# Kernel tuning notes

Measured on AMD Instinct MI355X. Metric: run time of the kernel, lower is better.

## Reference

```python
import jax, jax.numpy as jnp
import numpy as np

N_NODES = 100000
IN_CH, HID_CH, OUT_CH = 128, 128, 64
N_EDGES = 1600000


def gcn_conv(x, W, b, src, dst, num_nodes):
    """PyG GCNConv: x@W -> symmetric-normalized aggregation with self-loops -> +bias."""
    h = x @ W  # [N, out]
    loop = jnp.arange(num_nodes, dtype=src.dtype)
    src_a = jnp.concatenate([src, loop])  # add self-loops
    dst_a = jnp.concatenate([dst, loop])
    # degree of destination nodes over augmented edge set (edge_weight = 1)
    deg = jax.ops.segment_sum(jnp.ones_like(dst_a, dtype=h.dtype), dst_a,
                              num_segments=num_nodes)
    dis = jnp.where(deg > 0, jax.lax.rsqrt(jnp.maximum(deg, 1e-30)), 0.0)
    norm = dis[src_a] * dis[dst_a]  # [E+N]
    msg = h[src_a] * norm[:, None]  # gather + normalize
    out = jax.ops.segment_sum(msg, dst_a, num_segments=num_nodes)  # scatter-add
    return out + b


def setup_inputs() -> dict:
    key = jax.random.key(0)
    ks = jax.random.split(key, 9)
    x = jax.random.normal(ks[0], (N_NODES, IN_CH), dtype=jnp.float32)
    edge_index = jax.random.randint(ks[1], (2, N_EDGES), 0, N_NODES, dtype=jnp.int64)
    def glorot(k, fan_in, fan_out):
        s = np.sqrt(6.0 / (fan_in + fan_out)).astype(np.float32)
        return jax.random.uniform(k, (fan_in, fan_out), jnp.float32, -s, s)
    return {
        "x": x,
        "edge_index": edge_index,
        "W1": glorot(ks[2], IN_CH, HID_CH),
        "b1": jnp.zeros((HID_CH,), jnp.float32),
        "W2": glorot(ks[3], HID_CH, HID_CH),
        "b2": jnp.zeros((HID_CH,), jnp.float32),
        "Wo": glorot(ks[4], HID_CH, OUT_CH),
        "bo": jnp.zeros((OUT_CH,), jnp.float32),
    }


def reference(x, edge_index, W1, b1, W2, b2, Wo, bo):
    src, dst = edge_index[0], edge_index[1]
    n = x.shape[0]
    x1 = jax.nn.relu(gcn_conv(x, W1, b1, src, dst, n))
    x2 = jax.nn.relu(gcn_conv(x1, W2, b2, src, dst, n))
    return (x1 + x2) @ Wo + bo
```

## Files before the change

### kernel.cpp

```cpp
#include <hip/hip_runtime.h>
#include <hip/hip_fp16.h>

#define N_NODES 100000
#define N_EDGES 1600000
#define CH 128
#define OCH 64
#define NBUCKET 391
#define CAP 8192
#define BIN_CHUNK 4096
#define ZROW N_NODES
#define GG 782

typedef _Float16 half8 __attribute__((ext_vector_type(8)));
typedef float f32x4 __attribute__((ext_vector_type(4)));

__device__ __forceinline__ ushort f2h(float f) {
    _Float16 h = (_Float16)f;
    return *(ushort*)&h;
}

__device__ __forceinline__ uint pkadd(uint a, uint b) {
    __half2 r = __hadd2(*(__half2*)&a, *(__half2*)&b);
    return *(uint*)&r;
}

__device__ __forceinline__ uint4 pk4(uint4 a, uint4 b) {
    a.x = pkadd(a.x, b.x); a.y = pkadd(a.y, b.y);
    a.z = pkadd(a.z, b.z); a.w = pkadd(a.w, b.w);
    return a;
}

__device__ __forceinline__ int swz(int row, int k) {
    return row * 128 + ((((k >> 3) ^ (row & 15)) << 3) | (k & 7));
}


__global__ __launch_bounds__(512) void k_bin_prep(const int* __restrict__ src,
                                                  const int* __restrict__ dst,
                                                  int* __restrict__ bfill,
                                                  int* __restrict__ bin,
                                                  const float* __restrict__ W1,
                                                  const float* __restrict__ W2,
                                                  const float* __restrict__ Wo,
                                                  ushort* __restrict__ W1s,
                                                  ushort* __restrict__ W2s,
                                                  ushort* __restrict__ WoTs,
                                                  ushort* __restrict__ h) {
    __shared__ int hist[512];
    __shared__ int excl[512];
    __shared__ int wbase[512];
    __shared__ int cur[512];
    __shared__ int sbuf[BIN_CHUNK];
    __shared__ ushort sbkt[BIN_CHUNK];
    const int t = threadIdx.x;

    if (blockIdx.x >= NBUCKET) {
        int b = blockIdx.x - NBUCKET;
        if (b == 80) {
            if (t < CH) h[(size_t)ZROW * CH + t] = 0;
        } else {
            int i = b * 512 + t;
            if (i < 16384) {
                int k = i >> 7, n = i & 127;
                W1s[swz(n, k)] = f2h(W1[i]);
            } else if (i < 32768) {
                int j = i - 16384, k = j >> 7, n = j & 127;
                W2s[swz(n, k)] = f2h(W2[j]);
            } else {
                int j = i - 32768, k = j >> 6, n = j & 63;
                WoTs[swz(n, k)] = f2h(Wo[j]);
            }
        }
        return;
    }

    const int e0 = blockIdx.x * BIN_CHUNK;
    hist[t] = 0;
    __syncthreads();

    int ss[8], bb[8], dl[8];
#pragma unroll
    for (int j = 0; j < 8; ++j) {
        int e = e0 + j * 512 + t;
        bb[j] = -1;
        if (e < N_EDGES) {
            int s = src[e], d = dst[e];
            ss[j] = s; dl[j] = d & 255; bb[j] = d >> 8;
            atomicAdd(&hist[bb[j]], 1);
        }
    }
    __syncthreads();

    int v = hist[t];
    for (int off = 1; off < 512; off <<= 1) {
        int tv = (t >= off) ? hist[t - off] : 0;
        __syncthreads();
        hist[t] += tv;
        __syncthreads();
    }
    int ex = hist[t] - v;
    excl[t] = ex;
    cur[t] = ex;
    if (t < NBUCKET && v > 0) wbase[t] = atomicAdd(&bfill[t], v);
    __syncthreads();

#pragma unroll
    for (int j = 0; j < 8; ++j) {
        if (bb[j] >= 0) {
            int p = atomicAdd(&cur[bb[j]], 1);
            sbuf[p] = (ss[j] << 8) | dl[j];
            sbkt[p] = (ushort)bb[j];
        }
    }
    const int nloc = hist[511];
    __syncthreads();

    for (int i = t; i < nloc; i += 512) {
        int b = sbkt[i];
        bin[b * CAP + wbase[b] + (i - excl[b])] = sbuf[i];
    }
}


__global__ __launch_bounds__(512) void k_build(const int* __restrict__ bfill,
                                               const int* __restrict__ bin,
                                               int* __restrict__ esrc,
                                               int2* __restrict__ scnt,
                                               float* __restrict__ dis) {
    __shared__ int pre[512];
    __shared__ int cnt_l[256];
    __shared__ int cur_l[256];
    __shared__ int sortbuf[CAP];
    const int t = threadIdx.x;
    const int b = blockIdx.x;

    pre[t] = (t < NBUCKET) ? bfill[t] : 0;
    if (t < 256) cnt_l[t] = 0;
    __syncthreads();
    for (int off = 1; off < 512; off <<= 1) {
        int tv = (t >= off) ? pre[t - off] : 0;
        __syncthreads();
        pre[t] += tv;
        __syncthreads();
    }
    const int n = bfill[b];
    const int base = pre[b] - n;
    const int* brec = bin + b * CAP;

    for (int i = t; i < n; i += 512)
        atomicAdd(&cnt_l[brec[i] & 255], 1);
    __syncthreads();

    int v = (t < 256) ? cnt_l[t] : 0;
    for (int off = 1; off < 256; off <<= 1) {
        int tv = (t >= off && t < 256) ? cnt_l[t - off] : 0;
        __syncthreads();
        if (t < 256) cnt_l[t] += tv;
        __syncthreads();
    }
    if (t < 256) {
        int excl = cnt_l[t] - v;
        int node = b * 256 + t;
        if (node < N_NODES) {
            scnt[node] = make_int2(base + excl, v);
            dis[node] = rsqrtf((float)(v + 1));
        }
        cur_l[t] = excl;
    }
    __syncthreads();

    for (int i = t; i < n; i += 512) {
        int rec = brec[i];
        int p = atomicAdd(&cur_l[rec & 255], 1);
        sortbuf[p] = rec >> 8;
    }
    __syncthreads();
    for (int i = t; i < n; i += 512)
        esrc[base + i] = sortbuf[i];
}


template <typename IT>
__global__ __launch_bounds__(512) void k_gemm_mfma(const IT* __restrict__ A,
                                                   const ushort* __restrict__ Ws,
                                                   const float* __restrict__ dis,
                                                   ushort* __restrict__ out) {
    __shared__ ushort sB[128 * 128];
    __shared__ ushort sA[128 * 136];
    const int tid = threadIdx.x;
    const int row0 = blockIdx.x * 128;

    for (int i = tid; i < 2048; i += 512)
        ((float4*)sB)[i] = ((const float4*)Ws)[i];

    for (int i = tid; i < 4096; i += 512) {
        int m = i >> 5, u = i & 31, k4 = u << 2;
        int r = row0 + m;
        ushort4 pk = make_ushort4(0, 0, 0, 0);
        if (r < N_NODES) {
            if constexpr (sizeof(IT) == 4) {
                float4 a = ((const float4*)A)[r * 32 + u];
                pk = make_ushort4(f2h(a.x), f2h(a.y), f2h(a.z), f2h(a.w));
            } else {
                pk = ((const ushort4*)A)[r * 32 + u];
            }
        }
        *(ushort4*)&sA[swz(m, k4)] = pk;
    }
    __syncthreads();

    const int lane = tid & 63, wv = tid >> 6;
    const int mrow = lane & 15, quad = lane >> 4;
    f32x4 acc[8] = {};
#pragma unroll
    for (int kc = 0; kc < 4; ++kc) {
        int g = kc * 4 + quad;
        half8 a = *(const half8*)&sA[(wv * 16 + mrow) * 128 + ((g ^ mrow) << 3)];
#pragma unroll
        for (int nt = 0; nt < 8; ++nt) {
            half8 b = *(const half8*)&sB[(nt * 16 + mrow) * 128 + ((g ^ mrow) << 3)];
            acc[nt] = __builtin_amdgcn_mfma_f32_16x16x32_f16(a, b, acc[nt], 0, 0, 0);
        }
    }

    const int rbase4 = wv * 16 + quad * 4;
    float ds[4];
#pragma unroll
    for (int rg = 0; rg < 4; ++rg) {
        int r = row0 + rbase4 + rg;
        ds[rg] = (r < N_NODES) ? dis[r] : 0.f;
    }

    __syncthreads();
#pragma unroll
    for (int nt = 0; nt < 8; ++nt) {
#pragma unroll
        for (int rg = 0; rg < 4; ++rg)
            sA[(rbase4 + rg) * 136 + nt * 16 + mrow] = f2h(acc[nt][rg] * ds[rg]);
    }
    __syncthreads();

#pragma unroll
    for (int k = 0; k < 4; ++k) {
        int idx = tid + k * 512;
        int m = idx >> 4, c16 = idx & 15;
        int r = row0 + m;
        if (r < N_NODES) {
            uint4 vv = *(const uint4*)&sA[m * 136 + c16 * 8];
            ((uint4*)out)[(size_t)r * 16 + c16] = vv;
        }
    }
}


struct Ictx { int n; int grp; int s0, s1, s2, s3, s4, s5; };
struct Gt { uint4 t0, t1, t2, t3, t4, t5, slf; };

__device__ __forceinline__ Ictx idx_stage(const int* __restrict__ esrc, int off, int n, int q) {
    Ictx c; c.n = n;
    const int* ep = esrc + off;
    int r0 = ep[q], r1 = ep[q + 4], r2 = ep[q + 8];
    int r3 = ep[q + 12], r4 = ep[q + 16], r5 = ep[q + 20];
    bool grp = (q + 12 < n);
    bool ok = (n <= q + 24);
    c.grp = grp;
    c.s0 = (grp || q < n)      ? r0 : ZROW;
    c.s1 = (grp || q + 4 < n)  ? r1 : ZROW;
    c.s2 = (grp || q + 8 < n)  ? r2 : ZROW;
    c.s3 = grp                 ? r3 : ZROW;
    c.s4 = (grp && ok && q + 16 < n) ? r4 : ZROW;
    c.s5 = (grp && ok && q + 20 < n) ? r5 : ZROW;
    return c;
}

__device__ __forceinline__ Gt gather_stage(const Ictx& c, int v, int l,
                                           const uint4* __restrict__ h16) {
    Gt g;
    g.t0 = h16[(size_t)c.s0 * 16 + l];
    g.t1 = h16[(size_t)c.s1 * 16 + l];
    g.t2 = h16[(size_t)c.s2 * 16 + l];
    g.t3 = h16[(size_t)c.s3 * 16 + l];
    g.t4 = h16[(size_t)c.s4 * 16 + l];
    g.t5 = h16[(size_t)c.s5 * 16 + l];
    g.slf = h16[(size_t)v * 16 + l];
    return g;
}

__device__ __forceinline__ void acc_finish(const Gt& g, const Ictx& c, int v, int q, int l,
                                           const int* __restrict__ esrc, int off,
                                           const uint4* __restrict__ h16,
                                           float dsv, float4 b0, float4 b1,
                                           ushort* __restrict__ out) {
    uint4 aA = make_uint4(0, 0, 0, 0), aB = make_uint4(0, 0, 0, 0);
    aA = pk4(aA, g.t0);
    if (c.grp) aB = pk4(aB, g.t1); else aA = pk4(aA, g.t1);
    aA = pk4(aA, g.t2);
    if (c.grp) aB = pk4(aB, g.t3); else aA = pk4(aA, g.t3);
    aA = pk4(aA, g.t4);
    aA = pk4(aA, g.t5);
    if (c.n > q + 24) {
        const int* ep = esrc + off;
        int i = q + 16;
        for (; i + 12 < c.n; i += 16) {
            uint4 u0 = h16[(size_t)ep[i] * 16 + l];
            uint4 u1 = h16[(size_t)ep[i + 4] * 16 + l];
            uint4 u2 = h16[(size_t)ep[i + 8] * 16 + l];
            uint4 u3 = h16[(size_t)ep[i + 12] * 16 + l];
            aA = pk4(aA, u0); aB = pk4(aB, u1); aA = pk4(aA, u2); aB = pk4(aB, u3);
        }
        for (; i < c.n; i += 4) aA = pk4(aA, h16[(size_t)ep[i] * 16 + l]);
    }
    aA = pk4(aA, aB);
    aA.x = pkadd(aA.x, (uint)__shfl_xor((int)aA.x, 16));
    aA.y = pkadd(aA.y, (uint)__shfl_xor((int)aA.y, 16));
    aA.z = pkadd(aA.z, (uint)__shfl_xor((int)aA.z, 16));
    aA.w = pkadd(aA.w, (uint)__shfl_xor((int)aA.w, 16));
    aA.x = pkadd(aA.x, (uint)__shfl_xor((int)aA.x, 32));
    aA.y = pkadd(aA.y, (uint)__shfl_xor((int)aA.y, 32));
    aA.z = pkadd(aA.z, (uint)__shfl_xor((int)aA.z, 32));
    aA.w = pkadd(aA.w, (uint)__shfl_xor((int)aA.w, 32));

    if (q == 0) {
        aA = pk4(aA, g.slf);
        float2 a0 = __half22float2(*(__half2*)&aA.x);
        float2 a1 = __half22float2(*(__half2*)&aA.y);
        float2 a2 = __half22float2(*(__half2*)&aA.z);
        float2 a3 = __half22float2(*(__half2*)&aA.w);
        a0.x = fmaxf(a0.x * dsv + b0.x, 0.f); a0.y = fmaxf(a0.y * dsv + b0.y, 0.f);
        a1.x = fmaxf(a1.x * dsv + b0.z, 0.f); a1.y = fmaxf(a1.y * dsv + b0.w, 0.f);
        a2.x = fmaxf(a2.x * dsv + b1.x, 0.f); a2.y = fmaxf(a2.y * dsv + b1.y, 0.f);
        a3.x = fmaxf(a3.x * dsv + b1.z, 0.f); a3.y = fmaxf(a3.y * dsv + b1.w, 0.f);
        __half2 o0 = __float22half2_rn(a0);
        __half2 o1 = __float22half2_rn(a1);
        __half2 o2 = __float22half2_rn(a2);
        __half2 o3 = __float22half2_rn(a3);
        ((uint4*)out)[v * 16 + l] =
            make_uint4(*(uint*)&o0, *(uint*)&o1, *(uint*)&o2, *(uint*)&o3);
    }
}

__global__ __launch_bounds__(256) void k_agg(const int2* __restrict__ scnt,
                                             const int* __restrict__ esrc,
                                             const ushort* __restrict__ h,
                                             const float* __restrict__ dis,
                                             const float* __restrict__ bias,
                                             ushort* __restrict__ out) {
    const int w = threadIdx.x >> 6;
    const int vb = blockIdx.x * 16 + w * 4;
    const int lane = threadIdx.x & 63, q = lane >> 4, l = lane & 15;
    const uint4* h16 = (const uint4*)h;

    int2 m0 = scnt[vb], m1 = scnt[vb + 1], m2 = scnt[vb + 2], m3 = scnt[vb + 3];
    float d0 = dis[vb], d1 = dis[vb + 1], d2 = dis[vb + 2], d3 = dis[vb + 3];
    float4 b0 = ((const float4*)bias)[2 * l];
    float4 b1 = ((const float4*)bias)[2 * l + 1];

    Ictx c0 = idx_stage(esrc, m0.x, m0.y, q);
    Gt g0 = gather_stage(c0, vb, l, h16);
    Ictx c1 = idx_stage(esrc, m1.x, m1.y, q);
    Gt g1 = gather_stage(c1, vb + 1, l, h16);
    Ictx c2 = idx_stage(esrc, m2.x, m2.y, q);
    acc_finish(g0, c0, vb, q, l, esrc, m0.x, h16, d0, b0, b1, out);
    Gt g2 = gather_stage(c2, vb + 2, l, h16);
    Ictx c3 = idx_stage(esrc, m3.x, m3.y, q);
    acc_finish(g1, c1, vb + 1, q, l, esrc, m1.x, h16, d1, b0, b1, out);
    Gt g3 = gather_stage(c3, vb + 3, l, h16);
    acc_finish(g2, c2, vb + 2, q, l, esrc, m2.x, h16, d2, b0, b1, out);
    acc_finish(g3, c3, vb + 3, q, l, esrc, m3.x, h16, d3, b0, b1, out);
}


__global__ __launch_bounds__(512) void k_final_mfma(const ushort* __restrict__ x1,
                                                    const ushort* __restrict__ x2,
                                                    const ushort* __restrict__ Ws,
                                                    const float* __restrict__ bo,
                                                    float* __restrict__ out) {
    __shared__ ushort sB[64 * 128];
    __shared__ float sF[128 * 68];
    ushort* sA = (ushort*)sF;
    const int tid = threadIdx.x;
    const int row0 = blockIdx.x * 128;

    for (int i = tid; i < 1024; i += 512)
        ((float4*)sB)[i] = ((const float4*)Ws)[i];

    for (int i = tid; i < 4096; i += 512) {
        int m = i >> 5, u = i & 31, k4 = u << 2;
        int r = row0 + m;
        uint2 pk = make_uint2(0, 0);
        if (r < N_NODES) {
            uint2 ua = ((const uint2*)x1)[r * 32 + u];
            uint2 ub = ((const uint2*)x2)[r * 32 + u];
            __half2 s0 = __hadd2(*(__half2*)&ua.x, *(__half2*)&ub.x);
            __half2 s1 = __hadd2(*(__half2*)&ua.y, *(__half2*)&ub.y);
            pk = make_uint2(*(uint*)&s0, *(uint*)&s1);
        }
        *(uint2*)&sA[swz(m, k4)] = pk;
    }
    __syncthreads();

    const int lane = tid & 63, wv = tid >> 6;
    const int mrow = lane & 15, quad = lane >> 4;
    f32x4 acc[4] = {};
#pragma unroll
    for (int kc = 0; kc < 4; ++kc) {
        int g = kc * 4 + quad;
        half8 a = *(const half8*)&sA[(wv * 16 + mrow) * 128 + ((g ^ mrow) << 3)];
#pragma unroll
        for (int nt = 0; nt < 4; ++nt) {
            half8 b = *(const half8*)&sB[(nt * 16 + mrow) * 128 + ((g ^ mrow) << 3)];
            acc[nt] = __builtin_amdgcn_mfma_f32_16x16x32_f16(a, b, acc[nt], 0, 0, 0);
        }
    }

    const int rbase4 = wv * 16 + quad * 4;
    __syncthreads();
#pragma unroll
    for (int nt = 0; nt < 4; ++nt) {
        float bb = bo[nt * 16 + mrow];
#pragma unroll
        for (int rg = 0; rg < 4; ++rg)
            sF[(rbase4 + rg) * 68 + nt * 16 + mrow] = acc[nt][rg] + bb;
    }
    __syncthreads();

#pragma unroll
    for (int k = 0; k < 4; ++k) {
        int idx = tid + k * 512;
        int m = idx >> 4, c16 = idx & 15;
        int r = row0 + m;
        if (r < N_NODES) {
            uint4 vv = *(const uint4*)&sF[m * 68 + c16 * 4];
            ((uint4*)out)[(size_t)r * 16 + c16] = vv;
        }
    }
}


extern "C" void kernel_launch(void* const* d_in, const int* in_sizes, int n_in,
                              void* d_out, int out_size, void* d_ws, size_t ws_size,
                              hipStream_t stream) {
    const float* x  = (const float*)d_in[0];
    const int*   ei = (const int*)d_in[1];
    const int*   src = ei;
    const int*   dst = ei + N_EDGES;
    const float* W1 = (const float*)d_in[2];
    const float* b1 = (const float*)d_in[3];
    const float* W2 = (const float*)d_in[4];
    const float* b2 = (const float*)d_in[5];
    const float* Wo = (const float*)d_in[6];
    const float* bo = (const float*)d_in[7];
    float* out = (float*)d_out;

    char* ws = (char*)d_ws;
    int*    bfill  = (int*)ws;            ws += 2048;
    int2*   scnt   = (int2*)ws;           ws += 800000;
    float*  dis    = (float*)ws;          ws += 400000;
    int*    bin    = (int*)ws;            ws += (size_t)NBUCKET * CAP * 4;
    int*    esrc   = (int*)ws;            ws += (size_t)N_EDGES * 4;
    ushort* W1s    = (ushort*)ws;         ws += 32768;
    ushort* W2s    = (ushort*)ws;         ws += 32768;
    ushort* WoTs   = (ushort*)ws;         ws += 16384;
    ushort* h      = (ushort*)ws;         ws += (size_t)(N_NODES + 1) * CH * 2;
    ushort* x1     = (ushort*)ws;         ws += (size_t)N_NODES * CH * 2;
    ushort* x2     = (ushort*)ws;

    const int gA = N_NODES / 16;

    hipMemsetAsync(bfill, 0, 2048, stream);
    k_bin_prep<<<NBUCKET + 81, 512, 0, stream>>>(src, dst, bfill, bin,
                                                 W1, W2, Wo, W1s, W2s, WoTs, h);
    k_build<<<NBUCKET, 512, 0, stream>>>(bfill, bin, esrc, scnt, dis);

    k_gemm_mfma<float><<<GG, 512, 0, stream>>>(x, W1s, dis, h);
    k_agg<<<gA, 256, 0, stream>>>(scnt, esrc, h, dis, b1, x1);

    k_gemm_mfma<ushort><<<GG, 512, 0, stream>>>(x1, W2s, dis, h);
    k_agg<<<gA, 256, 0, stream>>>(scnt, esrc, h, dis, b2, x2);

    k_final_mfma<<<GG, 512, 0, stream>>>(x1, x2, WoTs, bo, out);
}
```

Before: 297.7 us.

## Fuse aggregation with following GEMMs to drop intermediate round-trips

The first aggregation kernel now also multiplies its 16-row output tile by W2 with MFMA and writes the dis-scaled h2 directly, which removes the separate second GEMM launch. The second aggregation fuses the x1 residual add and the output projection by Wo plus bias, which removes the x2 buffer and the final GEMM kernel. This saves two launches and the global write and reread of x2 and of x1 for the GEMM. In exchange the W2 and Wo fragments are read from global memory by every small block instead of being staged in LDS, and each block's MFMA work is small.

```diff
diff --git a/kernel.cpp b/kernel.cpp
--- a/kernel.cpp
+++ b/kernel.cpp
@@ -45,7 +45,8 @@
                                                   ushort* __restrict__ W1s,
                                                   ushort* __restrict__ W2s,
                                                   ushort* __restrict__ WoTs,
-                                                  ushort* __restrict__ h) {
+                                                  ushort* __restrict__ h,
+                                                  ushort* __restrict__ h2) {
     __shared__ int hist[512];
     __shared__ int excl[512];
     __shared__ int wbase[512];
@@ -57,7 +58,10 @@
     if (blockIdx.x >= NBUCKET) {
         int b = blockIdx.x - NBUCKET;
         if (b == 80) {
-            if (t < CH) h[(size_t)ZROW * CH + t] = 0;
+            if (t < CH) {
+                h[(size_t)ZROW * CH + t] = 0;
+                h2[(size_t)ZROW * CH + t] = 0;
+            }
         } else {
             int i = b * 512 + t;
             if (i < 16384) {
@@ -180,8 +184,7 @@
 }
 
 
-template <typename IT>
-__global__ __launch_bounds__(512) void k_gemm_mfma(const IT* __restrict__ A,
+__global__ __launch_bounds__(512) void k_gemm_mfma(const float* __restrict__ A,
                                                    const ushort* __restrict__ Ws,
                                                    const float* __restrict__ dis,
                                                    ushort* __restrict__ out) {
@@ -198,12 +201,8 @@
         int r = row0 + m;
         ushort4 pk = make_ushort4(0, 0, 0, 0);
         if (r < N_NODES) {
-            if constexpr (sizeof(IT) == 4) {
-                float4 a = ((const float4*)A)[r * 32 + u];
-                pk = make_ushort4(f2h(a.x), f2h(a.y), f2h(a.z), f2h(a.w));
-            } else {
-                pk = ((const ushort4*)A)[r * 32 + u];
-            }
+            float4 a = ((const float4*)A)[r * 32 + u];
+            pk = make_ushort4(f2h(a.x), f2h(a.y), f2h(a.z), f2h(a.w));
         }
         *(ushort4*)&sA[swz(m, k4)] = pk;
     }
@@ -286,11 +285,10 @@
     return g;
 }
 
-__device__ __forceinline__ void acc_finish(const Gt& g, const Ictx& c, int v, int q, int l,
-                                           const int* __restrict__ esrc, int off,
-                                           const uint4* __restrict__ h16,
-                                           float dsv, float4 b0, float4 b1,
-                                           ushort* __restrict__ out) {
+__device__ __forceinline__ uint4 acc_reduce(const Gt& g, const Ictx& c, int q, int l,
+                                            const int* __restrict__ esrc, int off,
+                                            const uint4* __restrict__ h16,
+                                            float dsv, float4 b0, float4 b1) {
     uint4 aA = make_uint4(0, 0, 0, 0), aB = make_uint4(0, 0, 0, 0);
     aA = pk4(aA, g.t0);
     if (c.grp) aB = pk4(aB, g.t1); else aA = pk4(aA, g.t1);
@@ -320,34 +318,38 @@
     aA.z = pkadd(aA.z, (uint)__shfl_xor((int)aA.z, 32));
     aA.w = pkadd(aA.w, (uint)__shfl_xor((int)aA.w, 32));
 
-    if (q == 0) {
-        aA = pk4(aA, g.slf);
-        float2 a0 = __half22float2(*(__half2*)&aA.x);
-        float2 a1 = __half22float2(*(__half2*)&aA.y);
-        float2 a2 = __half22float2(*(__half2*)&aA.z);
-        float2 a3 = __half22float2(*(__half2*)&aA.w);
-        a0.x = fmaxf(a0.x * dsv + b0.x, 0.f); a0.y = fmaxf(a0.y * dsv + b0.y, 0.f);
-        a1.x = fmaxf(a1.x * dsv + b0.z, 0.f); a1.y = fmaxf(a1.y * dsv + b0.w, 0.f);
-        a2.x = fmaxf(a2.x * dsv + b1.x, 0.f); a2.y = fmaxf(a2.y * dsv + b1.y, 0.f);
-        a3.x = fmaxf(a3.x * dsv + b1.z, 0.f); a3.y = fmaxf(a3.y * dsv + b1.w, 0.f);
-        __half2 o0 = __float22half2_rn(a0);
-        __half2 o1 = __float22half2_rn(a1);
-        __half2 o2 = __float22half2_rn(a2);
-        __half2 o3 = __float22half2_rn(a3);
-        ((uint4*)out)[v * 16 + l] =
-            make_uint4(*(uint*)&o0, *(uint*)&o1, *(uint*)&o2, *(uint*)&o3);
-    }
-}
-
-__global__ __launch_bounds__(256) void k_agg(const int2* __restrict__ scnt,
-                                             const int* __restrict__ esrc,
-                                             const ushort* __restrict__ h,
-                                             const float* __restrict__ dis,
-                                             const float* __restrict__ bias,
-                                             ushort* __restrict__ out) {
-    const int w = threadIdx.x >> 6;
-    const int vb = blockIdx.x * 16 + w * 4;
-    const int lane = threadIdx.x & 63, q = lane >> 4, l = lane & 15;
+    aA = pk4(aA, g.slf);
+    float2 a0 = __half22float2(*(__half2*)&aA.x);
+    float2 a1 = __half22float2(*(__half2*)&aA.y);
+    float2 a2 = __half22float2(*(__half2*)&aA.z);
+    float2 a3 = __half22float2(*(__half2*)&aA.w);
+    a0.x = fmaxf(a0.x * dsv + b0.x, 0.f); a0.y = fmaxf(a0.y * dsv + b0.y, 0.f);
+    a1.x = fmaxf(a1.x * dsv + b0.z, 0.f); a1.y = fmaxf(a1.y * dsv + b0.w, 0.f);
+    a2.x = fmaxf(a2.x * dsv + b1.x, 0.f); a2.y = fmaxf(a2.y * dsv + b1.y, 0.f);
+    a3.x = fmaxf(a3.x * dsv + b1.z, 0.f); a3.y = fmaxf(a3.y * dsv + b1.w, 0.f);
+    __half2 o0 = __float22half2_rn(a0);
+    __half2 o1 = __float22half2_rn(a1);
+    __half2 o2 = __float22half2_rn(a2);
+    __half2 o3 = __float22half2_rn(a3);
+    return make_uint4(*(uint*)&o0, *(uint*)&o1, *(uint*)&o2, *(uint*)&o3);
+}
+
+
+__global__ __launch_bounds__(256) void k_agg_gemm(const int2* __restrict__ scnt,
+                                                  const int* __restrict__ esrc,
+                                                  const ushort* __restrict__ h,
+                                                  const float* __restrict__ dis,
+                                                  const float* __restrict__ bias,
+                                                  const ushort* __restrict__ W2s,
+                                                  ushort* __restrict__ x1,
+                                                  ushort* __restrict__ h2) {
+    __shared__ ushort tile[16 * 128];
+    __shared__ ushort sBnc[16 * 136];
+    const int t = threadIdx.x;
+    const int w = t >> 6;
+    const int vb0 = blockIdx.x * 16;
+    const int vb = vb0 + w * 4;
+    const int lane = t & 63, q = lane >> 4, l = lane & 15;
     const uint4* h16 = (const uint4*)h;
 
     int2 m0 = scnt[vb], m1 = scnt[vb + 1], m2 = scnt[vb + 2], m3 = scnt[vb + 3];
@@ -360,80 +362,124 @@
     Ictx c1 = idx_stage(esrc, m1.x, m1.y, q);
     Gt g1 = gather_stage(c1, vb + 1, l, h16);
     Ictx c2 = idx_stage(esrc, m2.x, m2.y, q);
-    acc_finish(g0, c0, vb, q, l, esrc, m0.x, h16, d0, b0, b1, out);
+    uint4 ov = acc_reduce(g0, c0, q, l, esrc, m0.x, h16, d0, b0, b1);
+    if (q == 0) {
+        ((uint4*)x1)[(size_t)vb * 16 + l] = ov;
+        *(uint4*)&tile[swz(w * 4 + 0, l * 8)] = ov;
+    }
     Gt g2 = gather_stage(c2, vb + 2, l, h16);
     Ictx c3 = idx_stage(esrc, m3.x, m3.y, q);
-    acc_finish(g1, c1, vb + 1, q, l, esrc, m1.x, h16, d1, b0, b1, out);
+    ov = acc_reduce(g1, c1, q, l, esrc, m1.x, h16, d1, b0, b1);
+    if (q == 0) {
+        ((uint4*)x1)[(size_t)(vb + 1) * 16 + l] = ov;
+        *(uint4*)&tile[swz(w * 4 + 1, l * 8)] = ov;
+    }
     Gt g3 = gather_stage(c3, vb + 3, l, h16);
-    acc_finish(g2, c2, vb + 2, q, l, esrc, m2.x, h16, d2, b0, b1, out);
-    acc_finish(g3, c3, vb + 3, q, l, esrc, m3.x, h16, d3, b0, b1, out);
-}
-
-
-__global__ __launch_bounds__(512) void k_final_mfma(const ushort* __restrict__ x1,
-                                                    const ushort* __restrict__ x2,
-                                                    const ushort* __restrict__ Ws,
-                                                    const float* __restrict__ bo,
-                                                    float* __restrict__ out) {
-    __shared__ ushort sB[64 * 128];
-    __shared__ float sF[128 * 68];
-    ushort* sA = (ushort*)sF;
-    const int tid = threadIdx.x;
-    const int row0 = blockIdx.x * 128;
-
-    for (int i = tid; i < 1024; i += 512)
-        ((float4*)sB)[i] = ((const float4*)Ws)[i];
-
-    for (int i = tid; i < 4096; i += 512) {
-        int m = i >> 5, u = i & 31, k4 = u << 2;
-        int r = row0 + m;
-        uint2 pk = make_uint2(0, 0);
-        if (r < N_NODES) {
-            uint2 ua = ((const uint2*)x1)[r * 32 + u];
-            uint2 ub = ((const uint2*)x2)[r * 32 + u];
-            __half2 s0 = __hadd2(*(__half2*)&ua.x, *(__half2*)&ub.x);
-            __half2 s1 = __hadd2(*(__half2*)&ua.y, *(__half2*)&ub.y);
-            pk = make_uint2(*(uint*)&s0, *(uint*)&s1);
-        }
-        *(uint2*)&sA[swz(m, k4)] = pk;
-    }
-    __syncthreads();
-
-    const int lane = tid & 63, wv = tid >> 6;
+    ov = acc_reduce(g2, c2, q, l, esrc, m2.x, h16, d2, b0, b1);
+    if (q == 0) {
+        ((uint4*)x1)[(size_t)(vb + 2) * 16 + l] = ov;
+        *(uint4*)&tile[swz(w * 4 + 2, l * 8)] = ov;
+    }
+    ov = acc_reduce(g3, c3, q, l, esrc, m3.x, h16, d3, b0, b1);
+    if (q == 0) {
+        ((uint4*)x1)[(size_t)(vb + 3) * 16 + l] = ov;
+        *(uint4*)&tile[swz(w * 4 + 3, l * 8)] = ov;
+    }
+    __syncthreads();
+
     const int mrow = lane & 15, quad = lane >> 4;
-    f32x4 acc[4] = {};
+    f32x4 acc0 = {}, acc1 = {};
+    const int nt0 = 2 * w, nt1 = 2 * w + 1;
 #pragma unroll
     for (int kc = 0; kc < 4; ++kc) {
         int g = kc * 4 + quad;
-        half8 a = *(const half8*)&sA[(wv * 16 + mrow) * 128 + ((g ^ mrow) << 3)];
-#pragma unroll
-        for (int nt = 0; nt < 4; ++nt) {
-            half8 b = *(const half8*)&sB[(nt * 16 + mrow) * 128 + ((g ^ mrow) << 3)];
-            acc[nt] = __builtin_amdgcn_mfma_f32_16x16x32_f16(a, b, acc[nt], 0, 0, 0);
-        }
-    }
-
-    const int rbase4 = wv * 16 + quad * 4;
-    __syncthreads();
-#pragma unroll
-    for (int nt = 0; nt < 4; ++nt) {
-        float bb = bo[nt * 16 + mrow];
-#pragma unroll
-        for (int rg = 0; rg < 4; ++rg)
-            sF[(rbase4 + rg) * 68 + nt * 16 + mrow] = acc[nt][rg] + bb;
-    }
-    __syncthreads();
-
-#pragma unroll
-    for (int k = 0; k < 4; ++k) {
-        int idx = tid + k * 512;
-        int m = idx >> 4, c16 = idx & 15;
-        int r = row0 + m;
-        if (r < N_NODES) {
-            uint4 vv = *(const uint4*)&sF[m * 68 + c16 * 4];
-            ((uint4*)out)[(size_t)r * 16 + c16] = vv;
-        }
-    }
+        half8 a = *(const half8*)&tile[mrow * 128 + ((g ^ mrow) << 3)];
+        half8 bf0 = *(const half8*)&W2s[(nt0 * 16 + mrow) * 128 + ((g ^ mrow) << 3)];
+        half8 bf1 = *(const half8*)&W2s[(nt1 * 16 + mrow) * 128 + ((g ^ mrow) << 3)];
+        acc0 = __builtin_amdgcn_mfma_f32_16x16x32_f16(a, bf0, acc0, 0, 0, 0);
+        acc1 = __builtin_amdgcn_mfma_f32_16x16x32_f16(a, bf1, acc1, 0, 0, 0);
+    }
+    float ds[4];
+#pragma unroll
+    for (int rg = 0; rg < 4; ++rg)
+        ds[rg] = dis[vb0 + quad * 4 + rg];
+#pragma unroll
+    for (int rg = 0; rg < 4; ++rg) {
+        sBnc[(quad * 4 + rg) * 136 + nt0 * 16 + mrow] = f2h(acc0[rg] * ds[rg]);
+        sBnc[(quad * 4 + rg) * 136 + nt1 * 16 + mrow] = f2h(acc1[rg] * ds[rg]);
+    }
+    __syncthreads();
+
+    int row = t >> 4, c16 = t & 15;
+    uint4 vv = *(const uint4*)&sBnc[row * 136 + c16 * 8];
+    ((uint4*)h2)[(size_t)(vb0 + row) * 16 + c16] = vv;
+}
+
+
+__global__ __launch_bounds__(256) void k_agg_out(const int2* __restrict__ scnt,
+                                                 const int* __restrict__ esrc,
+                                                 const ushort* __restrict__ h2,
+                                                 const float* __restrict__ dis,
+                                                 const float* __restrict__ bias,
+                                                 const ushort* __restrict__ WoTs,
+                                                 const float* __restrict__ bo,
+                                                 const ushort* __restrict__ x1,
+                                                 float* __restrict__ out) {
+    __shared__ ushort tile[16 * 128];
+    __shared__ float sOut[16 * 68];
+    const int t = threadIdx.x;
+    const int w = t >> 6;
+    const int vb0 = blockIdx.x * 16;
+    const int vb = vb0 + w * 4;
+    const int lane = t & 63, q = lane >> 4, l = lane & 15;
+    const uint4* h16 = (const uint4*)h2;
+    const uint4* x1q = (const uint4*)x1;
+
+    int2 m0 = scnt[vb], m1 = scnt[vb + 1], m2 = scnt[vb + 2], m3 = scnt[vb + 3];
+    float d0 = dis[vb], d1 = dis[vb + 1], d2 = dis[vb + 2], d3 = dis[vb + 3];
+    float4 b0 = ((const float4*)bias)[2 * l];
+    float4 b1 = ((const float4*)bias)[2 * l + 1];
+
+    Ictx c0 = idx_stage(esrc, m0.x, m0.y, q);
+    Gt g0 = gather_stage(c0, vb, l, h16);
+    uint4 xr0 = x1q[(size_t)vb * 16 + l];
+    Ictx c1 = idx_stage(esrc, m1.x, m1.y, q);
+    Gt g1 = gather_stage(c1, vb + 1, l, h16);
+    uint4 xr1 = x1q[(size_t)(vb + 1) * 16 + l];
+    Ictx c2 = idx_stage(esrc, m2.x, m2.y, q);
+    uint4 ov = acc_reduce(g0, c0, q, l, esrc, m0.x, h16, d0, b0, b1);
+    if (q == 0) *(uint4*)&tile[swz(w * 4 + 0, l * 8)] = pk4(ov, xr0);
+    Gt g2 = gather_stage(c2, vb + 2, l, h16);
+    uint4 xr2 = x1q[(size_t)(vb + 2) * 16 + l];
+    Ictx c3 = idx_stage(esrc, m3.x, m3.y, q);
+    uint4 xr3 = x1q[(size_t)(vb + 3) * 16 + l];
+    ov = acc_reduce(g1, c1, q, l, esrc, m1.x, h16, d1, b0, b1);
+    if (q == 0) *(uint4*)&tile[swz(w * 4 + 1, l * 8)] = pk4(ov, xr1);
+    Gt g3 = gather_stage(c3, vb + 3, l, h16);
+    ov = acc_reduce(g2, c2, q, l, esrc, m2.x, h16, d2, b0, b1);
+    if (q == 0) *(uint4*)&tile[swz(w * 4 + 2, l * 8)] = pk4(ov, xr2);
+    ov = acc_reduce(g3, c3, q, l, esrc, m3.x, h16, d3, b0, b1);
+    if (q == 0) *(uint4*)&tile[swz(w * 4 + 3, l * 8)] = pk4(ov, xr3);
+    __syncthreads();
+
+    const int mrow = lane & 15, quad = lane >> 4;
+    f32x4 acc = {};
+#pragma unroll
+    for (int kc = 0; kc < 4; ++kc) {
+        int g = kc * 4 + quad;
+        half8 a = *(const half8*)&tile[mrow * 128 + ((g ^ mrow) << 3)];
+        half8 bf = *(const half8*)&WoTs[(w * 16 + mrow) * 128 + ((g ^ mrow) << 3)];
+        acc = __builtin_amdgcn_mfma_f32_16x16x32_f16(a, bf, acc, 0, 0, 0);
+    }
+    float bb = bo[w * 16 + mrow];
+#pragma unroll
+    for (int rg = 0; rg < 4; ++rg)
+        sOut[(quad * 4 + rg) * 68 + w * 16 + mrow] = acc[rg] + bb;
+    __syncthreads();
+
+    int row = t >> 4, c16 = t & 15;
+    uint4 vv = *(const uint4*)&sOut[row * 68 + c16 * 4];
+    ((uint4*)out)[(size_t)(vb0 + row) * 16 + c16] = vv;
 }
 
 
@@ -463,20 +509,18 @@
     ushort* WoTs   = (ushort*)ws;         ws += 16384;
     ushort* h      = (ushort*)ws;         ws += (size_t)(N_NODES + 1) * CH * 2;
     ushort* x1     = (ushort*)ws;         ws += (size_t)N_NODES * CH * 2;
-    ushort* x2     = (ushort*)ws;
+    ushort* h2     = (ushort*)ws;
 
     const int gA = N_NODES / 16;
 
     hipMemsetAsync(bfill, 0, 2048, stream);
     k_bin_prep<<<NBUCKET + 81, 512, 0, stream>>>(src, dst, bfill, bin,
-                                                 W1, W2, Wo, W1s, W2s, WoTs, h);
+                                                 W1, W2, Wo, W1s, W2s, WoTs, h, h2);
     k_build<<<NBUCKET, 512, 0, stream>>>(bfill, bin, esrc, scnt, dis);
 
-    k_gemm_mfma<float><<<GG, 512, 0, stream>>>(x, W1s, dis, h);
-    k_agg<<<gA, 256, 0, stream>>>(scnt, esrc, h, dis, b1, x1);
-
-    k_gemm_mfma<ushort><<<GG, 512, 0, stream>>>(x1, W2s, dis, h);
-    k_agg<<<gA, 256, 0, stream>>>(scnt, esrc, h, dis, b2, x2);
-
-    k_final_mfma<<<GG, 512, 0, stream>>>(x1, x2, WoTs, bo, out);
-}
+    k_gemm_mfma<<<GG, 512, 0, stream>>>(x, W1s, dis, h);
+
+    k_agg_gemm<<<gA, 256, 0, stream>>>(scnt, esrc, h, dis, b1, W2s, x1, h2);
+
+    k_agg_out<<<gA, 256, 0, stream>>>(scnt, esrc, h2, dis, b2, WoTs, bo, x1, out);
+}
```

Result: faster. 277.3 us, median of 2 (-6.8%).
